# Kernel tuning notes

Hardware: AMD Instinct MI355X
Metric: run time of the kernel (lower is better)

Reference implementation:

```python
import jax, jax.numpy as jnp
import numpy as np

B, S, E, H = 4, 2048, 1024, 16
DK = E // H  # 64


def setup_inputs() -> dict:
    key = jax.random.key(0)
    ks = jax.random.split(key, 11)
    s_in = 1.0 / np.sqrt(E)
    return {
        "query": jax.random.normal(ks[0], (B, S, E), jnp.float32),
        "key_": jax.random.normal(ks[1], (B, S, E), jnp.float32),
        "value": jax.random.normal(ks[2], (B, S, E), jnp.float32),
        # nn.Linear weights stored as [out, in]; applied as x @ W.T + b
        "Wq": jax.random.uniform(ks[3], (E, E), jnp.float32, -s_in, s_in),
        "bq": jax.random.uniform(ks[4], (E,), jnp.float32, -s_in, s_in),
        "Wk": jax.random.uniform(ks[5], (E, E), jnp.float32, -s_in, s_in),
        "bk": jax.random.uniform(ks[6], (E,), jnp.float32, -s_in, s_in),
        "Wv": jax.random.uniform(ks[7], (E, E), jnp.float32, -s_in, s_in),
        "bv": jax.random.uniform(ks[8], (E,), jnp.float32, -s_in, s_in),
        "Wo": jax.random.uniform(ks[9], (E, E), jnp.float32, -s_in, s_in),
        "bo": jax.random.uniform(ks[10], (E,), jnp.float32, -s_in, s_in),
    }


def reference(query, key_, value, Wq, bq, Wk, bk, Wv, bv, Wo, bo):
    scale = 1.0 / np.sqrt(DK).astype(np.float32)
    Q = query @ Wq.T + bq   # [B,S,E]
    K = key_ @ Wk.T + bk
    V = value @ Wv.T + bv
    # split heads: [B,S,H,DK] (slicing dim -1 into contiguous per-head chunks)
    Qh = Q.reshape(B, S, H, DK)
    Kh = K.reshape(B, S, H, DK)
    Vh = V.reshape(B, S, H, DK)
    scores = jnp.einsum('bqhd,bkhd->bhqk', Qh, Kh) * scale  # [B,H,S,S]
    probs = jax.nn.softmax(scores, axis=-1)
    ctx = jnp.einsum('bhqk,bkhd->bqhd', probs, Vh).reshape(B, S, E)
    out = ctx @ Wo.T + bo
    return out
```

## Files before the change

kernel.cpp:

```cpp
#include <hip/hip_runtime.h>
#include <stdint.h>
#include <stddef.h>

constexpr int BB = 4, SS = 2048, EE = 1024, HH = 16, DKH = 64;
constexpr int MM = BB * SS;
constexpr float SM_SCALE_LOG2 = 0.18033688011112042f;

typedef unsigned short u16;
typedef __attribute__((ext_vector_type(8))) short bf16x8;
typedef __attribute__((ext_vector_type(8))) unsigned short u16x8;
typedef __attribute__((ext_vector_type(4))) float f32x4;
typedef __attribute__((ext_vector_type(16))) float f32x16;
typedef __attribute__((ext_vector_type(2))) unsigned int u32x2;
typedef __attribute__((ext_vector_type(4))) unsigned int u32x4;

__device__ __forceinline__ u16 f2bf(float f) {
  unsigned u = __builtin_bit_cast(unsigned, f);
  u += 0x7FFFu + ((u >> 16) & 1u);
  return (u16)(u >> 16);
}

__device__ __forceinline__ unsigned pack2(float lo, float hi) {
  unsigned r;
  asm("v_cvt_pk_bf16_f32 %0, %1, %2" : "=v"(r) : "v"(lo), "v"(hi));
  return r;
}

__device__ __forceinline__ void gld16(const void* g, void* l) {
  __builtin_amdgcn_global_load_lds(
      (const __attribute__((address_space(1))) unsigned int*)g,
      (__attribute__((address_space(3))) unsigned int*)l, 16, 0, 0);
}

struct Cvt3 { const float* in[3]; u16* out[3]; };
struct Cvt4 { const float* in[4]; u16* out[4]; };

__global__ void cvt_bf16_x3(Cvt3 p, int n8) {
  int i = blockIdx.x * 256 + threadIdx.x;
  if (i >= n8) return;
  const int z = blockIdx.y;
  const float4* src = (const float4*)p.in[z] + (size_t)i * 2;
  float4 a = src[0], b = src[1];
  u16x8 v;
  v[0] = f2bf(a.x); v[1] = f2bf(a.y); v[2] = f2bf(a.z); v[3] = f2bf(a.w);
  v[4] = f2bf(b.x); v[5] = f2bf(b.y); v[6] = f2bf(b.z); v[7] = f2bf(b.w);
  *((u16x8*)p.out[z] + i) = v;
}

__global__ void cvt_bf16_x4(Cvt4 p, int n8) {
  int i = blockIdx.x * 256 + threadIdx.x;
  if (i >= n8) return;
  const int z = blockIdx.y;
  const float4* src = (const float4*)p.in[z] + (size_t)i * 2;
  float4 a = src[0], b = src[1];
  u16x8 v;
  v[0] = f2bf(a.x); v[1] = f2bf(a.y); v[2] = f2bf(a.z); v[3] = f2bf(a.w);
  v[4] = f2bf(b.x); v[5] = f2bf(b.y); v[6] = f2bf(b.z); v[7] = f2bf(b.w);
  *((u16x8*)p.out[z] + i) = v;
}

struct GemmPtrs {
  const u16* A[3];
  const u16* W[3];
  const float* bias[3];
  void* C[3];
  float scale[3];
  int mode[3];
};

__global__ __launch_bounds__(512, 2) void gemm256(GemmPtrs p, int M, int N, int K) {
  __shared__ __align__(16) u16 SA[3][256 * 32];
  __shared__ __align__(16) u16 SB[3][256 * 32];
  const int t = threadIdx.x, l = t & 63;
  const int w = t >> 6;
  const int lm = l & 15, lg = l >> 4;
  const int wm = w >> 2, wn = w & 3;
  const int z = blockIdx.z;
  const u16* A = p.A[z];
  const u16* W = p.W[z];
  const float* bias = p.bias[z];

  const int nwg = gridDim.x * gridDim.y;
  const int o = blockIdx.y * gridDim.x + blockIdx.x;
  const int cpx = nwg >> 3;
  const int sw = (o & 7) * cpx + (o >> 3);
  const int n0 = (sw % gridDim.x) * 256;
  const int m0 = (sw / gridDim.x) * 256;

  f32x4 acc[8][4];
  const f32x4 zero = {0.f, 0.f, 0.f, 0.f};
#pragma unroll
  for (int i = 0; i < 8; ++i)
#pragma unroll
    for (int j = 0; j < 4; ++j) acc[i][j] = zero;

  auto stage = [&](int buf, int kt) {
    const int k0 = kt * 32;
#pragma unroll
    for (int i = 0; i < 2; ++i) {
      const int cidx = i * 512 + t;
      const int row = cidx >> 2, pc = cidx & 3;
      const int lc = pc ^ (row & 3);
      const int dstoff = (i * 512 + (t & ~63)) * 16;
      gld16(A + (size_t)(m0 + row) * K + k0 + lc * 8, (char*)&SA[buf][0] + dstoff);
      gld16(W + (size_t)(n0 + row) * K + k0 + lc * 8, (char*)&SB[buf][0] + dstoff);
    }
  };

  stage(0, 0);
  stage(1, 1);
  int cb = 0;
  const int NT = K >> 5;
  const int rsw = (lg ^ (lm & 3)) * 8;
  for (int kt = 0; kt < NT; ++kt) {
    if (kt == NT - 1)
      asm volatile("s_waitcnt vmcnt(0)" ::: "memory");
    else
      asm volatile("s_waitcnt vmcnt(4)" ::: "memory");
    __builtin_amdgcn_s_barrier();
    const u16* Ac = &SA[cb][0];
    const u16* Bc = &SB[cb][0];
    bf16x8 a[8], b[4];
#pragma unroll
    for (int i = 0; i < 8; ++i)
      a[i] = *(const bf16x8*)(Ac + (wm * 128 + i * 16 + lm) * 32 + rsw);
#pragma unroll
    for (int j = 0; j < 4; ++j)
      b[j] = *(const bf16x8*)(Bc + (wn * 64 + j * 16 + lm) * 32 + rsw);
    if (kt + 2 < NT) {
      int sb = cb + 2;
      if (sb >= 3) sb -= 3;
      stage(sb, kt + 2);
    }
    __builtin_amdgcn_s_setprio(1);
#pragma unroll
    for (int i = 0; i < 8; ++i)
#pragma unroll
      for (int j = 0; j < 4; ++j)
        acc[i][j] = __builtin_amdgcn_mfma_f32_16x16x32_bf16(a[i], b[j], acc[i][j], 0, 0, 0);
    __builtin_amdgcn_s_setprio(0);
    cb = (cb == 2) ? 0 : cb + 1;
  }

  const float sc = p.scale[z];
  const int mode = p.mode[z];
#pragma unroll
  for (int i = 0; i < 8; ++i) {
    const int rbase = m0 + wm * 128 + i * 16 + lg * 4;
#pragma unroll
    for (int j = 0; j < 4; ++j) {
      const int col = n0 + wn * 64 + j * 16 + lm;
      const float bv = bias[col];
      float v[4];
#pragma unroll
      for (int r = 0; r < 4; ++r) v[r] = (acc[i][j][r] + bv) * sc;
      if (mode == 1) {
#pragma unroll
        for (int r = 0; r < 4; ++r)
          ((float*)p.C[z])[(size_t)(rbase + r) * N + col] = v[r];
      } else if (mode == 0) {
#pragma unroll
        for (int r = 0; r < 4; ++r)
          ((u16*)p.C[z])[(size_t)(rbase + r) * N + col] = f2bf(v[r]);
      } else {
        const int b = rbase >> 11, s = rbase & 2047;
        u16* dst = (u16*)p.C[z] +
                   ((size_t)((b * 16 + (col >> 6)) * 64 + (col & 63))) * SS + s;
        uint2 pk;
        pk.x = pack2(v[0], v[1]);
        pk.y = pack2(v[2], v[3]);
        *(uint2*)dst = pk;
      }
    }
  }
}

__global__ __launch_bounds__(256, 4) void attn_fwd3(const u16* __restrict__ Q,
                                                    const u16* __restrict__ K,
                                                    const u16* __restrict__ Vt,
                                                    u16* __restrict__ C) {
  __shared__ __align__(16) u16 Ks[2][64 * 64];
  __shared__ __align__(16) u16 Vs[2][64 * 64];

  const int t = threadIdx.x, l = t & 63, w = t >> 6;
  const int lq = l & 31, hi = l >> 5;
  const int q0 = blockIdx.x * 128;
  const int bh = blockIdx.y, bb = bh >> 4, hh = bh & 15;

  const u16* qp = Q + ((size_t)(bb * SS + q0 + w * 32 + lq)) * EE + hh * 64 + hi * 8;
  bf16x8 qf[4];
  qf[0] = *(const bf16x8*)(qp);
  qf[1] = *(const bf16x8*)(qp + 16);
  qf[2] = *(const bf16x8*)(qp + 32);
  qf[3] = *(const bf16x8*)(qp + 48);

  const u16* Kbase = K + (size_t)bb * SS * EE + hh * 64;
  const u16* Vbase = Vt + (size_t)bh * DKH * SS;

  f32x16 accA, accB;
  f32x16 z16;
#pragma unroll
  for (int i = 0; i < 16; ++i) { accA[i] = 0.f; accB[i] = 0.f; z16[i] = 0.f; }
  float lsum = 0.0f;

  auto stage = [&](int buf, int kt) {
#pragma unroll
    for (int i = 0; i < 2; ++i) {
      const int slot = i * 256 + t;
      const int row = slot >> 3, pc = slot & 7;
      const int lc = pc ^ (row & 7);
      const int lbyte = (i * 256 + (t & ~63)) * 16;
      gld16(Kbase + (size_t)(kt * 64 + row) * EE + lc * 8, (char*)&Ks[buf][0] + lbyte);
      gld16(Vbase + (size_t)row * SS + kt * 64 + lc * 8, (char*)&Vs[buf][0] + lbyte);
    }
  };

  auto mkfrag = [&](const f32x16& p, int base) -> bf16x8 {
    unsigned A0 = pack2(p[base + 0], p[base + 1]);
    unsigned A1 = pack2(p[base + 2], p[base + 3]);
    unsigned B0 = pack2(p[base + 4], p[base + 5]);
    unsigned B1 = pack2(p[base + 6], p[base + 7]);
    u32x2 r0 = __builtin_amdgcn_permlane32_swap(A0, B0, false, false);
    u32x2 r1 = __builtin_amdgcn_permlane32_swap(A1, B1, false, false);
    u32x4 fr;
    fr[0] = r0[0]; fr[1] = r1[0]; fr[2] = r0[1]; fr[3] = r1[1];
    return __builtin_bit_cast(bf16x8, fr);
  };

  stage(0, 0);
  __syncthreads();
  int cur = 0;
  for (int kt = 0; kt < SS / 64; ++kt) {
    if (kt + 1 < SS / 64) stage(cur ^ 1, kt + 1);
    const u16* Kc = &Ks[cur][0];
    const u16* Vc = &Vs[cur][0];

    f32x16 s0, s1;
    __builtin_amdgcn_s_setprio(1);
    {
      const int c = hi ^ (lq & 7);
      bf16x8 kf0 = *(const bf16x8*)(Kc + lq * 64 + c * 8);
      bf16x8 kf1 = *(const bf16x8*)(Kc + (32 + lq) * 64 + c * 8);
      s0 = __builtin_amdgcn_mfma_f32_32x32x16_bf16(kf0, qf[0], z16, 0, 0, 0);
      s1 = __builtin_amdgcn_mfma_f32_32x32x16_bf16(kf1, qf[0], z16, 0, 0, 0);
    }
#pragma unroll
    for (int m = 1; m < 4; ++m) {
      const int c = (2 * m + hi) ^ (lq & 7);
      bf16x8 kf0 = *(const bf16x8*)(Kc + lq * 64 + c * 8);
      bf16x8 kf1 = *(const bf16x8*)(Kc + (32 + lq) * 64 + c * 8);
      s0 = __builtin_amdgcn_mfma_f32_32x32x16_bf16(kf0, qf[m], s0, 0, 0, 0);
      s1 = __builtin_amdgcn_mfma_f32_32x32x16_bf16(kf1, qf[m], s1, 0, 0, 0);
    }
    __builtin_amdgcn_s_setprio(0);

#pragma unroll
    for (int i = 0; i < 16; ++i) {
      s0[i] = __builtin_amdgcn_exp2f(s0[i]);
      s1[i] = __builtin_amdgcn_exp2f(s1[i]);
    }
    float sa = 0.f, sb = 0.f, sc2 = 0.f, sd = 0.f;
#pragma unroll
    for (int i = 0; i < 8; ++i) {
      sa += s0[i]; sb += s0[i + 8];
      sc2 += s1[i]; sd += s1[i + 8];
    }
    lsum += (sa + sb) + (sc2 + sd);

    bf16x8 pf[4];
    pf[0] = mkfrag(s0, 0);
    pf[1] = mkfrag(s0, 8);
    pf[2] = mkfrag(s1, 0);
    pf[3] = mkfrag(s1, 8);

    __builtin_amdgcn_s_setprio(1);
#pragma unroll
    for (int s = 0; s < 4; ++s) {
      const int c = (2 * s + hi) ^ (lq & 7);
      bf16x8 vf0 = *(const bf16x8*)(Vc + lq * 64 + c * 8);
      bf16x8 vf1 = *(const bf16x8*)(Vc + (32 + lq) * 64 + c * 8);
      accA = __builtin_amdgcn_mfma_f32_32x32x16_bf16(vf0, pf[s], accA, 0, 0, 0);
      accB = __builtin_amdgcn_mfma_f32_32x32x16_bf16(vf1, pf[s], accB, 0, 0, 0);
    }
    __builtin_amdgcn_s_setprio(0);
    __syncthreads();
    cur ^= 1;
  }

  const float inv = 1.0f / (lsum + __shfl_xor(lsum, 32));
  char* Tw = (char*)&Ks[0][0] + w * 4096;
#pragma unroll
  for (int g = 0; g < 4; ++g) {
    uint2 pa, pb;
    pa.x = pack2(accA[4 * g + 0] * inv, accA[4 * g + 1] * inv);
    pa.y = pack2(accA[4 * g + 2] * inv, accA[4 * g + 3] * inv);
    pb.x = pack2(accB[4 * g + 0] * inv, accB[4 * g + 1] * inv);
    pb.y = pack2(accB[4 * g + 2] * inv, accB[4 * g + 3] * inv);
    const int sub = 8 * hi, sw = (lq & 7) << 4;
    *(uint2*)(Tw + lq * 128 + (((g) << 4) ^ sw) + sub) = pa;
    *(uint2*)(Tw + lq * 128 + (((4 + g) << 4) ^ sw) + sub) = pb;
  }
  const int qr0 = l >> 3, ch = l & 7;
#pragma unroll
  for (int ps = 0; ps < 4; ++ps) {
    const int qr = ps * 8 + qr0;
    u32x4 vv = *(const u32x4*)(Tw + qr * 128 + ((ch ^ (qr & 7)) << 4));
    u16* dst = C + ((size_t)(bb * SS + q0 + w * 32 + qr)) * EE + hh * 64 + ch * 8;
    *(u32x4*)dst = vv;
  }
}

extern "C" void kernel_launch(void* const* d_in, const int* in_sizes, int n_in,
                              void* d_out, int out_size, void* d_ws, size_t ws_size,
                              hipStream_t stream) {
  (void)in_sizes; (void)n_in; (void)out_size; (void)ws_size;
  const float* query = (const float*)d_in[0];
  const float* key_  = (const float*)d_in[1];
  const float* value = (const float*)d_in[2];
  const float* Wq = (const float*)d_in[3];
  const float* bq = (const float*)d_in[4];
  const float* Wk = (const float*)d_in[5];
  const float* bk = (const float*)d_in[6];
  const float* Wv = (const float*)d_in[7];
  const float* bv = (const float*)d_in[8];
  const float* Wo = (const float*)d_in[9];
  const float* bo = (const float*)d_in[10];

  char* ws = (char*)d_ws;
  const size_t SZX = (size_t)MM * EE * 2;
  const size_t SZW = (size_t)EE * EE * 2;
  u16* Xq  = (u16*)(ws + 0 * SZX);
  u16* Xk  = (u16*)(ws + 1 * SZX);
  u16* Xv  = (u16*)(ws + 2 * SZX);
  u16* Qb  = (u16*)(ws + 3 * SZX);
  u16* Kb  = (u16*)(ws + 4 * SZX);
  u16* Vtb = (u16*)(ws + 5 * SZX);
  u16* Cb  = (u16*)(ws + 6 * SZX);
  u16* Wqb = (u16*)(ws + 7 * SZX + 0 * SZW);
  u16* Wkb = (u16*)(ws + 7 * SZX + 1 * SZW);
  u16* Wvb = (u16*)(ws + 7 * SZX + 2 * SZW);
  u16* Wob = (u16*)(ws + 7 * SZX + 3 * SZW);

  const int n8x = MM * EE / 8;
  const int n8w = EE * EE / 8;

  Cvt3 cx{};
  cx.in[0] = query; cx.in[1] = key_; cx.in[2] = value;
  cx.out[0] = Xq; cx.out[1] = Xk; cx.out[2] = Xv;
  cvt_bf16_x3<<<dim3(n8x / 256, 3), 256, 0, stream>>>(cx, n8x);

  Cvt4 cw{};
  cw.in[0] = Wq; cw.in[1] = Wk; cw.in[2] = Wv; cw.in[3] = Wo;
  cw.out[0] = Wqb; cw.out[1] = Wkb; cw.out[2] = Wvb; cw.out[3] = Wob;
  cvt_bf16_x4<<<dim3(n8w / 256, 4), 256, 0, stream>>>(cw, n8w);

  GemmPtrs g{};
  g.A[0] = Xq; g.A[1] = Xk; g.A[2] = Xv;
  g.W[0] = Wqb; g.W[1] = Wkb; g.W[2] = Wvb;
  g.bias[0] = bq; g.bias[1] = bk; g.bias[2] = bv;
  g.C[0] = Qb; g.C[1] = Kb; g.C[2] = Vtb;
  g.scale[0] = SM_SCALE_LOG2; g.scale[1] = 1.0f; g.scale[2] = 1.0f;
  g.mode[0] = 0; g.mode[1] = 0; g.mode[2] = 2;
  gemm256<<<dim3(EE / 256, MM / 256, 3), 512, 0, stream>>>(g, MM, EE, EE);

  attn_fwd3<<<dim3(SS / 128, BB * HH), 256, 0, stream>>>(Qb, Kb, Vtb, Cb);

  GemmPtrs g2{};
  g2.A[0] = Cb; g2.W[0] = Wob; g2.bias[0] = bo; g2.C[0] = d_out;
  g2.scale[0] = 1.0f; g2.mode[0] = 1;
  gemm256<<<dim3(EE / 256, MM / 256, 1), 512, 0, stream>>>(g2, MM, EE, EE);
}
```

Before: 219.0 us.

## Restructure GEMM mainloop into 8-phase ping-pong schedule with 64-wide K tiles

Replaces the 3-stage, 32-wide-K GEMM pipeline with a double-buffered 64-wide-K tile. Each K-tile's compute is split into four phases interleaving LDS reads, partial global prefetches of the next tiles, barriers and MFMA bursts under sched_barrier control, in the style of HipKittens' 8-wave ping-pong. The aim is finer overlap of global loads with MFMA work and larger K per barrier. It adds many more barriers per tile and relies on careful vmcnt accounting, which risks stalls or ordering hazards.

After: 223.3 us. About the same (+2.0%).

```diff
diff --git a/kernel.cpp b/kernel.cpp
--- a/kernel.cpp
+++ b/kernel.cpp
@@ -68,9 +68,51 @@
   int mode[3];
 };
 
-__global__ __launch_bounds__(512, 2) void gemm256(GemmPtrs p, int M, int N, int K) {
-  __shared__ __align__(16) u16 SA[3][256 * 32];
-  __shared__ __align__(16) u16 SB[3][256 * 32];
+#define BARRIER() asm volatile("s_barrier" ::: "memory")
+
+#define RD_A(Ab, rg, kk) \
+  (*(const bf16x8*)((Ab) + aoff + (rg) * (16 * 64) + (((lg + 4 * (kk)) ^ csw) * 8)))
+#define RD_B(Bb, j, kk) \
+  (*(const bf16x8*)((Bb) + boff + (j) * (16 * 64) + (((lg + 4 * (kk)) ^ csw) * 8)))
+
+#define PHASE(Ab, Bb, q, STAGE, POST)                                              \
+  do {                                                                             \
+    __builtin_amdgcn_sched_barrier(0);                                             \
+    bf16x8 a00 = RD_A(Ab, 2 * (q), 0), a01 = RD_A(Ab, 2 * (q), 1);                 \
+    bf16x8 a10 = RD_A(Ab, 2 * (q) + 1, 0), a11 = RD_A(Ab, 2 * (q) + 1, 1);         \
+    if ((q) == 0) {                                                                \
+      _Pragma("unroll") for (int j = 0; j < 4; ++j) {                              \
+        bfr[j][0] = RD_B(Bb, j, 0);                                                \
+        bfr[j][1] = RD_B(Bb, j, 1);                                                \
+      }                                                                            \
+    }                                                                              \
+    STAGE;                                                                         \
+    __builtin_amdgcn_sched_barrier(0);                                             \
+    BARRIER();                                                                     \
+    asm volatile("s_waitcnt lgkmcnt(0)" ::: "memory");                             \
+    __builtin_amdgcn_sched_barrier(0);                                             \
+    __builtin_amdgcn_s_setprio(1);                                                 \
+    _Pragma("unroll") for (int j = 0; j < 4; ++j) {                                \
+      acc[2 * (q)][j] =                                                            \
+          __builtin_amdgcn_mfma_f32_16x16x32_bf16(a00, bfr[j][0], acc[2 * (q)][j], 0, 0, 0); \
+      acc[2 * (q) + 1][j] =                                                        \
+          __builtin_amdgcn_mfma_f32_16x16x32_bf16(a10, bfr[j][0], acc[2 * (q) + 1][j], 0, 0, 0); \
+    }                                                                              \
+    _Pragma("unroll") for (int j = 0; j < 4; ++j) {                                \
+      acc[2 * (q)][j] =                                                            \
+          __builtin_amdgcn_mfma_f32_16x16x32_bf16(a01, bfr[j][1], acc[2 * (q)][j], 0, 0, 0); \
+      acc[2 * (q) + 1][j] =                                                        \
+          __builtin_amdgcn_mfma_f32_16x16x32_bf16(a11, bfr[j][1], acc[2 * (q) + 1][j], 0, 0, 0); \
+    }                                                                              \
+    __builtin_amdgcn_s_setprio(0);                                                 \
+    __builtin_amdgcn_sched_barrier(0);                                             \
+    POST;                                                                          \
+    BARRIER();                                                                     \
+  } while (0)
+
+__global__ __launch_bounds__(512, 2) void gemm8p(GemmPtrs p, int M, int N, int K) {
+  __shared__ __align__(16) u16 SA[2][256 * 64];
+  __shared__ __align__(16) u16 SB[2][256 * 64];
   const int t = threadIdx.x, l = t & 63;
   const int w = t >> 6;
   const int lm = l & 15, lg = l >> 4;
@@ -94,52 +136,56 @@
 #pragma unroll
     for (int j = 0; j < 4; ++j) acc[i][j] = zero;
 
-  auto stage = [&](int buf, int kt) {
-    const int k0 = kt * 32;
+  auto stA = [&](int kt, int h) {
 #pragma unroll
     for (int i = 0; i < 2; ++i) {
-      const int cidx = i * 512 + t;
-      const int row = cidx >> 2, pc = cidx & 3;
-      const int lc = pc ^ (row & 3);
-      const int dstoff = (i * 512 + (t & ~63)) * 16;
-      gld16(A + (size_t)(m0 + row) * K + k0 + lc * 8, (char*)&SA[buf][0] + dstoff);
-      gld16(W + (size_t)(n0 + row) * K + k0 + lc * 8, (char*)&SB[buf][0] + dstoff);
+      const int ci = i * 512 + t;
+      const int row = ci >> 3, s = ci & 7;
+      const int c = s ^ (row & 7);
+      gld16(A + (size_t)(m0 + h * 128 + row) * K + kt * 64 + c * 8,
+            (char*)&SA[kt & 1][h * 128 * 64] + (i * 512 + (t & ~63)) * 16);
     }
   };
-
-  stage(0, 0);
-  stage(1, 1);
-  int cb = 0;
-  const int NT = K >> 5;
-  const int rsw = (lg ^ (lm & 3)) * 8;
-  for (int kt = 0; kt < NT; ++kt) {
-    if (kt == NT - 1)
-      asm volatile("s_waitcnt vmcnt(0)" ::: "memory");
-    else
-      asm volatile("s_waitcnt vmcnt(4)" ::: "memory");
-    __builtin_amdgcn_s_barrier();
-    const u16* Ac = &SA[cb][0];
-    const u16* Bc = &SB[cb][0];
-    bf16x8 a[8], b[4];
-#pragma unroll
-    for (int i = 0; i < 8; ++i)
-      a[i] = *(const bf16x8*)(Ac + (wm * 128 + i * 16 + lm) * 32 + rsw);
-#pragma unroll
-    for (int j = 0; j < 4; ++j)
-      b[j] = *(const bf16x8*)(Bc + (wn * 64 + j * 16 + lm) * 32 + rsw);
-    if (kt + 2 < NT) {
-      int sb = cb + 2;
-      if (sb >= 3) sb -= 3;
-      stage(sb, kt + 2);
-    }
-    __builtin_amdgcn_s_setprio(1);
-#pragma unroll
-    for (int i = 0; i < 8; ++i)
-#pragma unroll
-      for (int j = 0; j < 4; ++j)
-        acc[i][j] = __builtin_amdgcn_mfma_f32_16x16x32_bf16(a[i], b[j], acc[i][j], 0, 0, 0);
-    __builtin_amdgcn_s_setprio(0);
-    cb = (cb == 2) ? 0 : cb + 1;
+  auto stB = [&](int kt, int h) {
+#pragma unroll
+    for (int i = 0; i < 2; ++i) {
+      const int ci = i * 512 + t;
+      const int row = ci >> 3, s = ci & 7;
+      const int c = s ^ (row & 7);
+      gld16(W + (size_t)(n0 + h * 128 + row) * K + kt * 64 + c * 8,
+            (char*)&SB[kt & 1][h * 128 * 64] + (i * 512 + (t & ~63)) * 16);
+    }
+  };
+
+  const int aoff = (wm * 128 + lm) * 64;
+  const int boff = (wn * 64 + lm) * 64;
+  const int csw = lm & 7;
+
+  bf16x8 bfr[4][2];
+
+  stA(0, 0); stA(0, 1); stB(0, 0); stB(0, 1); stB(1, 0); stB(1, 1);
+  asm volatile("s_waitcnt vmcnt(4)" ::: "memory");
+  BARRIER();
+
+  const int NIT = K >> 7;
+  const u16* A0 = &SA[0][0];
+  const u16* B0 = &SB[0][0];
+  const u16* A1 = &SA[1][0];
+  const u16* B1 = &SB[1][0];
+  for (int it = 0; it < NIT; ++it) {
+    const int t0 = 2 * it;
+    const bool nx = (it + 1 < NIT);
+    PHASE(A0, B0, 0, stA(t0 + 1, 0), );
+    PHASE(A0, B0, 1, stA(t0 + 1, 1), );
+    PHASE(A0, B0, 2, if (nx) stB(t0 + 2, 0), );
+    PHASE(A0, B0, 3, if (nx) stB(t0 + 2, 1),
+          if (nx) asm volatile("s_waitcnt vmcnt(4)" ::: "memory");
+          else    asm volatile("s_waitcnt vmcnt(0)" ::: "memory"); );
+    PHASE(A1, B1, 0, if (nx) stA(t0 + 2, 0), );
+    PHASE(A1, B1, 1, if (nx) stA(t0 + 2, 1), );
+    PHASE(A1, B1, 2, if (nx) stB(t0 + 3, 0), );
+    PHASE(A1, B1, 3, if (nx) stB(t0 + 3, 1),
+          if (nx) asm volatile("s_waitcnt vmcnt(4)" ::: "memory"); );
   }
 
   const float sc = p.scale[z];
@@ -361,12 +407,12 @@
   g.C[0] = Qb; g.C[1] = Kb; g.C[2] = Vtb;
   g.scale[0] = SM_SCALE_LOG2; g.scale[1] = 1.0f; g.scale[2] = 1.0f;
   g.mode[0] = 0; g.mode[1] = 0; g.mode[2] = 2;
-  gemm256<<<dim3(EE / 256, MM / 256, 3), 512, 0, stream>>>(g, MM, EE, EE);
+  gemm8p<<<dim3(EE / 256, MM / 256, 3), 512, 0, stream>>>(g, MM, EE, EE);
 
   attn_fwd3<<<dim3(SS / 128, BB * HH), 256, 0, stream>>>(Qb, Kb, Vtb, Cb);
 
   GemmPtrs g2{};
   g2.A[0] = Cb; g2.W[0] = Wob; g2.bias[0] = bo; g2.C[0] = d_out;
   g2.scale[0] = 1.0f; g2.mode[0] = 1;
-  gemm256<<<dim3(EE / 256, MM / 256, 1), 512, 0, stream>>>(g2, MM, EE, EE);
-}
+  gemm8p<<<dim3(EE / 256, MM / 256, 1), 512, 0, stream>>>(g2, MM, EE, EE);
+}
```
